# Kernel tuning notes

Hardware: AMD Instinct MI355X
Metric: run time of the kernel (lower is better)

Reference implementation:

```python
import jax, jax.numpy as jnp
import numpy as np

NUM_AGENTS = 50
NUM_SLOTS = 7
SLOT_DIM = 64
HIDDEN = 128
TOPK = 3
ITERS = 3


def _ln(x, eps=1e-5):
    m = x.mean(axis=-1, keepdims=True)
    v = ((x - m) ** 2).mean(axis=-1, keepdims=True)
    return (x - m) / jnp.sqrt(v + eps)


def setup_inputs() -> dict:
    key = jax.random.key(0)
    ks = jax.random.split(key, 20)
    r = lambda i, shape, s=0.05: jax.random.normal(ks[i], shape, dtype=jnp.float32) * s
    B = 32
    return {
        'images': jax.random.normal(ks[0], (B, 3, 32, 32), dtype=jnp.float32),
        'slot_noise': jax.random.normal(ks[1], (B, NUM_SLOTS, SLOT_DIM), dtype=jnp.float32),
        'enc_w0': r(2, (64, 3, 3, 3)), 'enc_b0': jnp.zeros((64,), jnp.float32),
        'enc_w': r(3, (3, 64, 64, 3, 3)), 'enc_b': jnp.zeros((3, 64), jnp.float32),
        'enc_wo': r(4, (256, 64, 3, 3)), 'enc_bo': jnp.zeros((256,), jnp.float32),
        'wk': r(5, (256, SLOT_DIM)), 'wv': r(6, (256, SLOT_DIM)), 'wq': r(7, (SLOT_DIM, SLOT_DIM)),
        'gru_wi': r(8, (SLOT_DIM, 3 * SLOT_DIM)), 'gru_wh': r(9, (SLOT_DIM, 3 * SLOT_DIM)),
        'gru_b': jnp.zeros((3 * SLOT_DIM,), jnp.float32),
        'mlp_w1': r(10, (SLOT_DIM, 128)), 'mlp_b1': jnp.zeros((128,), jnp.float32),
        'mlp_w2': r(11, (128, SLOT_DIM)), 'mlp_b2': jnp.zeros((SLOT_DIM,), jnp.float32),
        'slots_mu': r(12, (1, NUM_SLOTS, SLOT_DIM), 1.0),
        'slots_logsigma': jnp.zeros((1, NUM_SLOTS, SLOT_DIM), jnp.float32),
        'est_we': r(13, (NUM_AGENTS, SLOT_DIM, 32)), 'est_wd': r(14, (NUM_AGENTS, 32, SLOT_DIM)),
        'ag_win': r(15, (NUM_AGENTS, SLOT_DIM, 256)), 'ag_bin': jnp.zeros((NUM_AGENTS, 256), jnp.float32),
        'ag_wblk': r(16, (NUM_AGENTS, 3, 256, 256)), 'ag_bblk': jnp.zeros((NUM_AGENTS, 3, 256), jnp.float32),
        'ag_wout': r(17, (NUM_AGENTS, 256, HIDDEN)), 'ag_bout': jnp.zeros((NUM_AGENTS, HIDDEN), jnp.float32),
    }


def reference(images, slot_noise, enc_w0, enc_b0, enc_w, enc_b, enc_wo, enc_bo,
              wk, wv, wq, gru_wi, gru_wh, gru_b, mlp_w1, mlp_b1, mlp_w2, mlp_b2,
              slots_mu, slots_logsigma, est_we, est_wd,
              ag_win, ag_bin, ag_wblk, ag_bblk, ag_wout, ag_bout):
    conv = lambda x, w, b: jax.lax.conv_general_dilated(
        x, w, (1, 1), 'SAME', dimension_numbers=('NCHW', 'OIHW', 'NCHW')) + b[None, :, None, None]
    # ---- CNN encoder: 4 hidden conv layers + projection to 256 channels ----
    x = jax.nn.relu(conv(images, enc_w0, enc_b0))
    for i in range(enc_w.shape[0]):
        x = jax.nn.relu(conv(x, enc_w[i], enc_b[i]))
    feats = conv(x, enc_wo, enc_bo)                         # (B, 256, H, W)
    B, Df, H, W = feats.shape
    inputs = feats.transpose(0, 2, 3, 1).reshape(B, H * W, Df)  # (B, N, 256)
    inputs_n = _ln(inputs)
    k = inputs_n @ wk                                       # (B, N, Ds)
    v = inputs_n @ wv
    # ---- stochastic slot init ----
    slots = slots_mu + slot_noise * jnp.exp(slots_logsigma)  # (B, S, Ds)
    scale = SLOT_DIM ** -0.5
    # ---- slot attention, 3 iterations ----
    for _ in range(ITERS):
        prev = slots
        q = _ln(slots) @ wq * scale                         # (B, S, Ds)
        attn = jax.nn.softmax(jnp.einsum('bnd,bsd->bns', k, q), axis=-1) + 1e-8
        attn_w = attn / attn.sum(axis=1, keepdims=True)     # weighted mean over N
        updates = jnp.einsum('bns,bnd->bsd', attn_w, v)
        gi = updates @ gru_wi + gru_b
        gh = prev @ gru_wh
        zi, ri, ni = jnp.split(gi, 3, axis=-1)
        zh, rh, nh = jnp.split(gh, 3, axis=-1)
        z = jax.nn.sigmoid(zi + zh)
        rr = jax.nn.sigmoid(ri + rh)
        n = jnp.tanh(ni + rr * nh)
        slots = (1.0 - z) * n + z * prev
        slots = slots + (jax.nn.relu(_ln(slots) @ mlp_w1 + mlp_b1) @ mlp_w2 + mlp_b2)
    # ---- per-slot VAE-estimator scores (neg reconstruction error) ----
    lat = jnp.einsum('bsd,adz->bsaz', slots, est_we)        # (B, S, A, Z)
    recon = jnp.einsum('bsaz,azd->bsad', lat, est_wd)       # (B, S, A, Ds)
    scores = -((recon - slots[:, :, None, :]) ** 2).sum(axis=-1)  # (B, S, A)
    # ---- top-k agent selection per slot ----
    _, idx = jax.lax.top_k(scores, TOPK)                    # (B, S, K) int32
    ids = idx.reshape(-1)                                   # (T,) T = B*S*K
    tok = jnp.broadcast_to(slots[:, :, None, :], (B, NUM_SLOTS, TOPK, SLOT_DIM)).reshape(-1, SLOT_DIM)
    # ---- batched expert (residual MLP) dispatch via gathered params ----
    h = jax.nn.relu(jnp.einsum('td,tdh->th', tok, ag_win[ids]) + ag_bin[ids])  # (T, 256)
    for i in range(ag_wblk.shape[1]):
        h = jax.nn.relu(h + jnp.einsum('th,thg->tg', h, ag_wblk[ids, i]) + ag_bblk[ids, i])
    out = jnp.einsum('th,tho->to', h, ag_wout[ids]) + ag_bout[ids]             # (T, 128)
    hidden_labels = out.reshape(B, NUM_SLOTS * TOPK * HIDDEN)                  # concat mode: (B, 2688)
    return hidden_labels
```

## Files before the change

### kernel.cpp

```cpp
#include <hip/hip_runtime.h>
#include <hip/hip_bf16.h>
#include <math.h>

#define DEV __device__ __forceinline__

DEV double wred_sumd(double v) {
#pragma unroll
  for (int m = 1; m < 64; m <<= 1) v += __shfl_xor(v, m, 64);
  return v;
}

template <int CIN, bool RELU>
__global__ __launch_bounds__(256) void conv3x3_kernel(
    const float* __restrict__ in, const float* __restrict__ wgt,
    const float* __restrict__ bias, float* __restrict__ out,
    int cout_total, int cb_count) {
  constexpr int CHUNK = (CIN < 16) ? CIN : 16;
  __shared__ float s_in[6 * CHUNK * 35];
  __shared__ float s_w[CHUNK * 9 * 64];
  int bx = blockIdx.x;
  int cb = bx % cb_count;
  bx /= cb_count;
  int hb = bx & 7;
  int b = bx >> 3;
  int co_base = cb * 64;
  int t = threadIdx.x;
  int w_g = t & 7, co_g = (t >> 3) & 7, h_l = t >> 6;
  int h0 = hb * 4;
  int w0 = w_g * 4;
  float acc[8][4];
#pragma unroll
  for (int j = 0; j < 8; ++j)
#pragma unroll
    for (int ww = 0; ww < 4; ++ww) acc[j][ww] = 0.f;

  for (int cc = 0; cc < CIN; cc += CHUNK) {
    __syncthreads();
    for (int i = t; i < 6 * CHUNK * 32; i += 256) {
      int r = i / (CHUNK * 32);
      int c = (i >> 5) % CHUNK;
      int w = i & 31;
      int gh = h0 - 1 + r;
      float v = 0.f;
      if (gh >= 0 && gh < 32) v = in[((b * CIN + cc + c) * 32 + gh) * 32 + w];
      s_in[(r * CHUNK + c) * 35 + w + 1] = v;
    }
    for (int i = t; i < 6 * CHUNK; i += 256) {
      s_in[i * 35] = 0.f;
      s_in[i * 35 + 33] = 0.f;
    }
    for (int i = t; i < CHUNK * 9 * 64; i += 256) {
      int co = i / (CHUNK * 9);
      int rem = i % (CHUNK * 9);
      s_w[rem * 64 + co] = wgt[((co_base + co) * CIN + cc) * 9 + rem];
    }
    __syncthreads();
    for (int c = 0; c < CHUNK; ++c) {
#pragma unroll
      for (int kh = 0; kh < 3; ++kh) {
        const float* ip = &s_in[((h_l + kh) * CHUNK + c) * 35 + w0];
        float ivs[6];
#pragma unroll
        for (int j = 0; j < 6; ++j) ivs[j] = ip[j];
        const float* wp = &s_w[(c * 9 + kh * 3) * 64 + co_g * 8];
#pragma unroll
        for (int kw = 0; kw < 3; ++kw) {
          float4 wa = *(const float4*)(wp + kw * 64);
          float4 wb = *(const float4*)(wp + kw * 64 + 4);
          float wr[8] = {wa.x, wa.y, wa.z, wa.w, wb.x, wb.y, wb.z, wb.w};
#pragma unroll
          for (int j = 0; j < 8; ++j)
#pragma unroll
            for (int ww = 0; ww < 4; ++ww)
              acc[j][ww] = fmaf(ivs[kw + ww], wr[j], acc[j][ww]);
        }
      }
    }
  }
  int h = h0 + h_l;
#pragma unroll
  for (int j = 0; j < 8; ++j) {
    int co = co_base + co_g * 8 + j;
    float bv = bias[co];
    float4 o;
    o.x = acc[j][0] + bv;
    o.y = acc[j][1] + bv;
    o.z = acc[j][2] + bv;
    o.w = acc[j][3] + bv;
    if (RELU) {
      o.x = fmaxf(o.x, 0.f);
      o.y = fmaxf(o.y, 0.f);
      o.z = fmaxf(o.z, 0.f);
      o.w = fmaxf(o.w, 0.f);
    }
    *(float4*)(&out[((b * cout_total + co) * 32 + h) * 32 + w0]) = o;
  }
}

__global__ __launch_bounds__(256) void conv5_ln_kv_fused(
    const float* __restrict__ in,
    const float* __restrict__ wgt,
    const float* __restrict__ bias,
    const float* __restrict__ wk, const float* __restrict__ wv,
    float* __restrict__ kout, float* __restrict__ vout) {
  int bp = blockIdx.x;
  int b = bp >> 6, pt = bp & 63;
  int h = pt >> 1, w0 = (pt & 1) * 16;
  int t = threadIdx.x;
  int px = t & 15, cg = t >> 4;

  __shared__ float s_w[2 * 9 * 256];
  __shared__ float s_in[2][3][20];
  __shared__ float s_red[16][17];
  __shared__ float s_m[16], s_isd[16];
  __shared__ float s_xn[16][257];

  float acc[16];
#pragma unroll
  for (int j = 0; j < 16; ++j) acc[j] = 0.f;

  for (int cc = 0; cc < 64; cc += 2) {
    __syncthreads();
    for (int i = t; i < 2 * 9 * 256; i += 256) {
      int co = i & 255;
      int rem = i >> 8;
      int c = rem / 9, k = rem % 9;
      s_w[(c * 9 + k) * 256 + co] = wgt[(co * 64 + cc + c) * 9 + k];
    }
    for (int i = t; i < 2 * 3 * 18; i += 256) {
      int c = i / 54;
      int r = (i / 18) % 3;
      int cw = i % 18;
      int gh = h + r - 1;
      int gw = w0 + cw - 1;
      float v = 0.f;
      if (gh >= 0 && gh < 32 && gw >= 0 && gw < 32)
        v = in[((b * 64 + c + cc) * 32 + gh) * 32 + gw];
      s_in[c][r][cw] = v;
    }
    __syncthreads();
#pragma unroll
    for (int c = 0; c < 2; ++c) {
#pragma unroll
      for (int kh = 0; kh < 3; ++kh) {
        float iv[3];
#pragma unroll
        for (int kw = 0; kw < 3; ++kw) iv[kw] = s_in[c][kh][px + kw];
        const float* wp = &s_w[(c * 9 + kh * 3) * 256 + cg * 16];
#pragma unroll
        for (int kw = 0; kw < 3; ++kw) {
#pragma unroll
          for (int j = 0; j < 16; ++j)
            acc[j] = fmaf(iv[kw], wp[kw * 256 + j], acc[j]);
        }
      }
    }
  }
#pragma unroll
  for (int j = 0; j < 16; ++j) acc[j] += bias[cg * 16 + j];
  float psum = 0.f;
#pragma unroll
  for (int j = 0; j < 16; ++j) psum += acc[j];
  s_red[px][cg] = psum;
  __syncthreads();
  if (t < 16) {
    float m = 0.f;
    for (int g = 0; g < 16; ++g) m += s_red[t][g];
    s_m[t] = m * (1.f / 256.f);
  }
  __syncthreads();
  float m = s_m[px];
  float vp = 0.f;
#pragma unroll
  for (int j = 0; j < 16; ++j) {
    float dv = acc[j] - m;
    vp += dv * dv;
  }
  s_red[px][cg] = vp;
  __syncthreads();
  if (t < 16) {
    float v = 0.f;
    for (int g = 0; g < 16; ++g) v += s_red[t][g];
    s_isd[t] = 1.f / sqrtf(v * (1.f / 256.f) + 1e-5f);
  }
  __syncthreads();
  float isd = s_isd[px];
#pragma unroll
  for (int j = 0; j < 16; ++j) s_xn[px][cg * 16 + j] = (acc[j] - m) * isd;
  __syncthreads();
  const float* wb = (cg < 8) ? wk : wv;
  int d0 = (cg & 7) * 8;
  float a2[8];
#pragma unroll
  for (int j = 0; j < 8; ++j) a2[j] = 0.f;
  for (int c = 0; c < 256; ++c) {
    float xv = s_xn[px][c];
    const float* wr = &wb[c * 64 + d0];
#pragma unroll
    for (int j = 0; j < 8; ++j) a2[j] = fmaf(xv, wr[j], a2[j]);
  }
  int p = h * 32 + w0 + px;
  float* ob = (cg < 8) ? kout : vout;
#pragma unroll
  for (int j = 0; j < 8; ++j) ob[(b * 1024 + p) * 64 + d0 + j] = a2[j];
}

__global__ __launch_bounds__(64) void slot_init(
    const float* __restrict__ mu, const float* __restrict__ logsig,
    const float* __restrict__ noise, const float* __restrict__ wq,
    double* __restrict__ slots, double* __restrict__ qbuf) {
  int bs = blockIdx.x;
  int d = threadIdx.x;
  int sr = bs % 7;
  __shared__ double ln[64], red[64];
  double s = (double)mu[sr * 64 + d] +
             (double)noise[bs * 64 + d] * exp((double)logsig[sr * 64 + d]);
  slots[bs * 64 + d] = s;
  red[d] = s;
  __syncthreads();
  for (int st = 32; st > 0; st >>= 1) {
    if (d < st) red[d] += red[d + st];
    __syncthreads();
  }
  double m = red[0] * (1.0 / 64.0);
  __syncthreads();
  double dv = s - m;
  red[d] = dv * dv;
  __syncthreads();
  for (int st = 32; st > 0; st >>= 1) {
    if (d < st) red[d] += red[d + st];
    __syncthreads();
  }
  double isd = 1.0 / sqrt(red[0] * (1.0 / 64.0) + 1e-5);
  __syncthreads();
  ln[d] = dv * isd;
  __syncthreads();
  double q = 0.0;
  for (int dd = 0; dd < 64; ++dd) q += ln[dd] * (double)wq[dd * 64 + d];
  qbuf[bs * 64 + d] = q * 0.125;
}

__global__ __launch_bounds__(256) void attn_softmax(
    const float* __restrict__ kbuf, const double* __restrict__ qbuf,
    double* __restrict__ attw) {
  int idx = blockIdx.x * 256 + threadIdx.x;
  if (idx >= 32 * 1024) return;
  int b = idx >> 10;
  int n = idx & 1023;
  double l[7];
  for (int s = 0; s < 7; ++s) {
    double acc = 0.0;
    for (int d = 0; d < 64; ++d)
      acc += (double)kbuf[idx * 64 + d] * qbuf[(b * 7 + s) * 64 + d];
    l[s] = acc;
  }
  double mx = l[0];
  for (int s = 1; s < 7; ++s) mx = fmax(mx, l[s]);
  double sum = 0.0;
  for (int s = 0; s < 7; ++s) {
    l[s] = exp(l[s] - mx);
    sum += l[s];
  }
  double inv = 1.0 / sum;
  for (int s = 0; s < 7; ++s)
    attw[(size_t)(b * 7 + s) * 1024 + n] = l[s] * inv + 1e-8;
}

__global__ __launch_bounds__(256) void attn_update_slot(
    const double* __restrict__ attw, const float* __restrict__ vbuf,
    const float* __restrict__ gwi, const float* __restrict__ gwh,
    const float* __restrict__ gb, const float* __restrict__ w1,
    const float* __restrict__ b1, const float* __restrict__ w2,
    const float* __restrict__ b2, const float* __restrict__ wq,
    double* __restrict__ slots, double* __restrict__ qbuf) {
  int bs = blockIdx.x;
  int b = bs / 7;
  int t = threadIdx.x;
  int d = t & 63, q = t >> 6;
  __shared__ double s_aw[1024];
  __shared__ double part[4][64];
  __shared__ double red256[256];
  __shared__ double s_u[64], s_p[64], s_ln[64], s_h[128];
  for (int i = t; i < 1024; i += 256) s_aw[i] = attw[(size_t)bs * 1024 + i];
  __syncthreads();
  double ps = 0.0;
#pragma unroll
  for (int k = 0; k < 4; ++k) ps += s_aw[q * 256 + k * 64 + d];
  red256[t] = ps;
  double acc = 0.0;
  const float* vb = vbuf + ((size_t)(b * 1024 + q * 256)) * 64 + d;
  for (int n = 0; n < 256; ++n)
    acc += s_aw[q * 256 + n] * (double)vb[(size_t)n * 64];
  part[q][d] = acc;
  __syncthreads();
  for (int st = 128; st > 0; st >>= 1) {
    if (t < st) red256[t] += red256[t + st];
    __syncthreads();
  }
  double asum = red256[0];
  if (t < 64) {
    double u = ((part[0][d] + part[1][d]) + part[2][d]) + part[3][d];
    s_u[d] = u / asum;
    s_p[d] = slots[bs * 64 + d];
  }
  __syncthreads();
  if (t >= 64) return;
  double giz = (double)gb[d], gir = (double)gb[64 + d], gin = (double)gb[128 + d];
  double ghz = 0.0, ghr = 0.0, ghn = 0.0;
  for (int dd = 0; dd < 64; ++dd) {
    double uu = s_u[dd], pp = s_p[dd];
    giz += uu * (double)gwi[dd * 192 + d];
    gir += uu * (double)gwi[dd * 192 + 64 + d];
    gin += uu * (double)gwi[dd * 192 + 128 + d];
    ghz += pp * (double)gwh[dd * 192 + d];
    ghr += pp * (double)gwh[dd * 192 + 64 + d];
    ghn += pp * (double)gwh[dd * 192 + 128 + d];
  }
  double z = 1.0 / (1.0 + exp(-(giz + ghz)));
  double r = 1.0 / (1.0 + exp(-(gir + ghr)));
  double nn = tanh(gin + r * ghn);
  double sv = (1.0 - z) * nn + z * s_p[d];
  double m = wred_sumd(sv) * (1.0 / 64.0);
  double dv = sv - m;
  double var = wred_sumd(dv * dv) * (1.0 / 64.0);
  s_ln[d] = dv / sqrt(var + 1e-5);
  double h0 = (double)b1[d], h1 = (double)b1[64 + d];
  for (int dd = 0; dd < 64; ++dd) {
    double lv = s_ln[dd];
    h0 += lv * (double)w1[dd * 128 + d];
    h1 += lv * (double)w1[dd * 128 + 64 + d];
  }
  s_h[d] = fmax(h0, 0.0);
  s_h[64 + d] = fmax(h1, 0.0);
  double o = (double)b2[d];
  for (int e = 0; e < 128; ++e) o += s_h[e] * (double)w2[e * 64 + d];
  double s2 = sv + o;
  slots[bs * 64 + d] = s2;
  double m2 = wred_sumd(s2) * (1.0 / 64.0);
  double dv2 = s2 - m2;
  double var2 = wred_sumd(dv2 * dv2) * (1.0 / 64.0);
  s_ln[d] = dv2 / sqrt(var2 + 1e-5);
  double qv = 0.0;
  for (int dd = 0; dd < 64; ++dd) qv += s_ln[dd] * (double)wq[dd * 64 + d];
  qbuf[bs * 64 + d] = qv * 0.125;
}

__global__ __launch_bounds__(256) void scores_naive(
    const double* __restrict__ slots, const float* __restrict__ we,
    const float* __restrict__ wd, double* __restrict__ sc) {
  int idx = blockIdx.x * 256 + threadIdx.x;
  if (idx >= 224 * 50) return;
  int a = idx % 50, bs = idx / 50;
  double lat[32];
  for (int z = 0; z < 32; ++z) {
    double acc = 0.0;
    for (int dd = 0; dd < 64; ++dd)
      acc += slots[bs * 64 + dd] * (double)we[(a * 64 + dd) * 32 + z];
    lat[z] = acc;
  }
  double sum = 0.0;
  for (int dd = 0; dd < 64; ++dd) {
    double rec = 0.0;
    for (int z = 0; z < 32; ++z) rec += lat[z] * (double)wd[(a * 32 + z) * 64 + dd];
    double df = rec - slots[bs * 64 + dd];
    sum += df * df;
  }
  sc[idx] = -sum;
}

__global__ __launch_bounds__(256) void topk_naive(const double* __restrict__ sc,
                                                  int* __restrict__ topk) {
  int bs = blockIdx.x * 256 + threadIdx.x;
  if (bs >= 224) return;
  int chosen[3];
  for (int r = 0; r < 3; ++r) {
    double best = -1e300;
    int bi = -1;
    for (int a = 0; a < 50; ++a) {
      bool skip = false;
      for (int rr = 0; rr < r; ++rr)
        if (chosen[rr] == a) skip = true;
      if (skip) continue;
      double v = sc[bs * 50 + a];
      if (v > best) {
        best = v;
        bi = a;
      }
    }
    chosen[r] = bi;
    topk[bs * 3 + r] = bi;
  }
}

__global__ __launch_bounds__(256) void expert_naive(
    const int* __restrict__ topk, const double* __restrict__ slots,
    const float* __restrict__ win, const float* __restrict__ bin,
    const float* __restrict__ wblk, const float* __restrict__ bblk,
    const float* __restrict__ wout, const float* __restrict__ bout,
    float* __restrict__ outp) {
  int ti = blockIdx.x;
  int a = topk[ti];
  int bs = ti / 3;
  int t = threadIdx.x;
  __shared__ double tok[64], ha[256], hb[256];
  if (t < 64) tok[t] = slots[bs * 64 + t];
  __syncthreads();
  double acc = (double)bin[a * 256 + t];
  for (int dd = 0; dd < 64; ++dd)
    acc += tok[dd] * (double)win[(a * 64 + dd) * 256 + t];
  ha[t] = fmax(acc, 0.0);
  __syncthreads();
  double* cur = ha;
  double* nxt = hb;
  for (int i = 0; i < 3; ++i) {
    double a2 = cur[t] + (double)bblk[(a * 3 + i) * 256 + t];
    for (int hh = 0; hh < 256; ++hh)
      a2 += cur[hh] * (double)wblk[((a * 3 + i) * 256 + hh) * 256 + t];
    nxt[t] = fmax(a2, 0.0);
    __syncthreads();
    double* tmp = cur;
    cur = nxt;
    nxt = tmp;
  }
  if (t < 128) {
    double a3 = (double)bout[a * 128 + t];
    for (int hh = 0; hh < 256; ++hh)
      a3 += cur[hh] * (double)wout[(a * 256 + hh) * 128 + t];
    outp[ti * 128 + t] = (float)a3;
  }
}

extern "C" void kernel_launch(void* const* d_in, const int* in_sizes, int n_in,
                              void* d_out, int out_size, void* d_ws,
                              size_t ws_size, hipStream_t stream) {
  (void)in_sizes; (void)n_in; (void)out_size; (void)ws_size;
  const float* images = (const float*)d_in[0];
  const float* noise = (const float*)d_in[1];
  const float* enc_w0 = (const float*)d_in[2];
  const float* enc_b0 = (const float*)d_in[3];
  const float* enc_w = (const float*)d_in[4];
  const float* enc_b = (const float*)d_in[5];
  const float* enc_wo = (const float*)d_in[6];
  const float* enc_bo = (const float*)d_in[7];
  const float* wk = (const float*)d_in[8];
  const float* wv = (const float*)d_in[9];
  const float* wq = (const float*)d_in[10];
  const float* gru_wi = (const float*)d_in[11];
  const float* gru_wh = (const float*)d_in[12];
  const float* gru_b = (const float*)d_in[13];
  const float* mlp_w1 = (const float*)d_in[14];
  const float* mlp_b1 = (const float*)d_in[15];
  const float* mlp_w2 = (const float*)d_in[16];
  const float* mlp_b2 = (const float*)d_in[17];
  const float* mu = (const float*)d_in[18];
  const float* logsig = (const float*)d_in[19];
  const float* est_we = (const float*)d_in[20];
  const float* est_wd = (const float*)d_in[21];
  const float* ag_win = (const float*)d_in[22];
  const float* ag_bin = (const float*)d_in[23];
  const float* ag_wblk = (const float*)d_in[24];
  const float* ag_bblk = (const float*)d_in[25];
  const float* ag_wout = (const float*)d_in[26];
  const float* ag_bout = (const float*)d_in[27];

  double* dws = (double*)d_ws;
  double* slots = dws;
  double* qbuf = slots + 14336;
  double* upd = qbuf + 14336;
  double* attw = upd + 14336;
  double* sc = attw + 229376;
  int* topk = (int*)(sc + 11200);
  float* xA = (float*)(topk + 1024);
  float* xB = xA + 2097152;
  float* vbuf = xB + 2097152;

  conv3x3_kernel<3, true><<<256, 256, 0, stream>>>(images, enc_w0, enc_b0, xA, 64, 1);
  conv3x3_kernel<64, true><<<256, 256, 0, stream>>>(xA, enc_w, enc_b, xB, 64, 1);
  conv3x3_kernel<64, true><<<256, 256, 0, stream>>>(xB, enc_w + 36864, enc_b + 64, xA, 64, 1);
  conv3x3_kernel<64, true><<<256, 256, 0, stream>>>(xA, enc_w + 73728, enc_b + 128, xB, 64, 1);
  conv5_ln_kv_fused<<<2048, 256, 0, stream>>>(xB, enc_wo, enc_bo, wk, wv, xA, vbuf);
  slot_init<<<224, 64, 0, stream>>>(mu, logsig, noise, wq, slots, qbuf);
  for (int it = 0; it < 3; ++it) {
    attn_softmax<<<128, 256, 0, stream>>>(xA, qbuf, attw);
    attn_update_slot<<<224, 256, 0, stream>>>(attw, vbuf, gru_wi, gru_wh,
                                              gru_b, mlp_w1, mlp_b1, mlp_w2,
                                              mlp_b2, wq, slots, qbuf);
  }
  scores_naive<<<44, 256, 0, stream>>>(slots, est_we, est_wd, sc);
  topk_naive<<<1, 256, 0, stream>>>(sc, topk);
  expert_naive<<<672, 256, 0, stream>>>(topk, slots, ag_win, ag_bin, ag_wblk,
                                        ag_bblk, ag_wout, ag_bout,
                                        (float*)d_out);
}
```

Before: 1.755 ms.

## Coalesce conv5 weight loads, stage q in LDS, widen slot-update blocks

The conv5 weight staging now reads global weights contiguously per output channel and stores them into a padded LDS layout (stride 257). This trades bank conflicts on the store for coalesced global reads. attn_softmax caches the per-batch queries in shared memory and loads each key row as float4 vectors, avoiding repeated strided global reads. attn_update_slot uses 512 threads so the attention-weighted value sum is split eight ways, which shortens each thread's serial loop but adds reduction and sync cost.

```diff
diff --git a/kernel.cpp b/kernel.cpp
--- a/kernel.cpp
+++ b/kernel.cpp
@@ -109,7 +109,7 @@
   int t = threadIdx.x;
   int px = t & 15, cg = t >> 4;
 
-  __shared__ float s_w[2 * 9 * 256];
+  __shared__ float s_w[18 * 257];
   __shared__ float s_in[2][3][20];
   __shared__ float s_red[16][17];
   __shared__ float s_m[16], s_isd[16];
@@ -121,11 +121,9 @@
 
   for (int cc = 0; cc < 64; cc += 2) {
     __syncthreads();
-    for (int i = t; i < 2 * 9 * 256; i += 256) {
-      int co = i & 255;
-      int rem = i >> 8;
-      int c = rem / 9, k = rem % 9;
-      s_w[(c * 9 + k) * 256 + co] = wgt[(co * 64 + cc + c) * 9 + k];
+    for (int i = t; i < 256 * 18; i += 256) {
+      int co = i / 18, rem = i % 18;
+      s_w[rem * 257 + co] = wgt[co * 576 + cc * 9 + rem];
     }
     for (int i = t; i < 2 * 3 * 18; i += 256) {
       int c = i / 54;
@@ -146,12 +144,12 @@
         float iv[3];
 #pragma unroll
         for (int kw = 0; kw < 3; ++kw) iv[kw] = s_in[c][kh][px + kw];
-        const float* wp = &s_w[(c * 9 + kh * 3) * 256 + cg * 16];
+        const float* wp = &s_w[(c * 9 + kh * 3) * 257 + cg * 16];
 #pragma unroll
         for (int kw = 0; kw < 3; ++kw) {
 #pragma unroll
           for (int j = 0; j < 16; ++j)
-            acc[j] = fmaf(iv[kw], wp[kw * 256 + j], acc[j]);
+            acc[j] = fmaf(iv[kw], wp[kw * 257 + j], acc[j]);
         }
       }
     }
@@ -243,30 +241,48 @@
 __global__ __launch_bounds__(256) void attn_softmax(
     const float* __restrict__ kbuf, const double* __restrict__ qbuf,
     double* __restrict__ attw) {
-  int idx = blockIdx.x * 256 + threadIdx.x;
-  if (idx >= 32 * 1024) return;
-  int b = idx >> 10;
-  int n = idx & 1023;
+  int bx = blockIdx.x;
+  int b = bx >> 2;
+  int n0 = (bx & 3) * 256;
+  int t = threadIdx.x;
+  int n = n0 + t;
+  __shared__ double s_q[448];
+  for (int i = t; i < 448; i += 256) s_q[i] = qbuf[b * 448 + i];
+  __syncthreads();
+  float4 kr[16];
+  const float4* kp = (const float4*)(kbuf + ((size_t)(b * 1024 + n)) * 64);
+#pragma unroll
+  for (int i = 0; i < 16; ++i) kr[i] = kp[i];
   double l[7];
+#pragma unroll
   for (int s = 0; s < 7; ++s) {
     double acc = 0.0;
-    for (int d = 0; d < 64; ++d)
-      acc += (double)kbuf[idx * 64 + d] * qbuf[(b * 7 + s) * 64 + d];
+    const double* qs = &s_q[s * 64];
+#pragma unroll
+    for (int i = 0; i < 16; ++i) {
+      acc += (double)kr[i].x * qs[i * 4 + 0];
+      acc += (double)kr[i].y * qs[i * 4 + 1];
+      acc += (double)kr[i].z * qs[i * 4 + 2];
+      acc += (double)kr[i].w * qs[i * 4 + 3];
+    }
     l[s] = acc;
   }
   double mx = l[0];
+#pragma unroll
   for (int s = 1; s < 7; ++s) mx = fmax(mx, l[s]);
   double sum = 0.0;
+#pragma unroll
   for (int s = 0; s < 7; ++s) {
     l[s] = exp(l[s] - mx);
     sum += l[s];
   }
   double inv = 1.0 / sum;
+#pragma unroll
   for (int s = 0; s < 7; ++s)
     attw[(size_t)(b * 7 + s) * 1024 + n] = l[s] * inv + 1e-8;
 }
 
-__global__ __launch_bounds__(256) void attn_update_slot(
+__global__ __launch_bounds__(512) void attn_update_slot(
     const double* __restrict__ attw, const float* __restrict__ vbuf,
     const float* __restrict__ gwi, const float* __restrict__ gwh,
     const float* __restrict__ gb, const float* __restrict__ w1,
@@ -278,28 +294,26 @@
   int t = threadIdx.x;
   int d = t & 63, q = t >> 6;
   __shared__ double s_aw[1024];
-  __shared__ double part[4][64];
-  __shared__ double red256[256];
+  __shared__ double part[8][64];
+  __shared__ double red[512];
   __shared__ double s_u[64], s_p[64], s_ln[64], s_h[128];
-  for (int i = t; i < 1024; i += 256) s_aw[i] = attw[(size_t)bs * 1024 + i];
-  __syncthreads();
-  double ps = 0.0;
-#pragma unroll
-  for (int k = 0; k < 4; ++k) ps += s_aw[q * 256 + k * 64 + d];
-  red256[t] = ps;
+  for (int i = t; i < 1024; i += 512) s_aw[i] = attw[(size_t)bs * 1024 + i];
+  __syncthreads();
+  red[t] = s_aw[t] + s_aw[t + 512];
   double acc = 0.0;
-  const float* vb = vbuf + ((size_t)(b * 1024 + q * 256)) * 64 + d;
-  for (int n = 0; n < 256; ++n)
-    acc += s_aw[q * 256 + n] * (double)vb[(size_t)n * 64];
+  const float* vb = vbuf + ((size_t)(b * 1024 + q * 128)) * 64 + d;
+  for (int nn = 0; nn < 128; ++nn)
+    acc += s_aw[q * 128 + nn] * (double)vb[(size_t)nn * 64];
   part[q][d] = acc;
   __syncthreads();
-  for (int st = 128; st > 0; st >>= 1) {
-    if (t < st) red256[t] += red256[t + st];
-    __syncthreads();
-  }
-  double asum = red256[0];
+  for (int st = 256; st > 0; st >>= 1) {
+    if (t < st) red[t] += red[t + st];
+    __syncthreads();
+  }
+  double asum = red[0];
   if (t < 64) {
-    double u = ((part[0][d] + part[1][d]) + part[2][d]) + part[3][d];
+    double u = ((part[0][d] + part[1][d]) + (part[2][d] + part[3][d])) +
+               ((part[4][d] + part[5][d]) + (part[6][d] + part[7][d]));
     s_u[d] = u / asum;
     s_p[d] = slots[bs * 64 + d];
   }
@@ -318,8 +332,8 @@
   }
   double z = 1.0 / (1.0 + exp(-(giz + ghz)));
   double r = 1.0 / (1.0 + exp(-(gir + ghr)));
-  double nn = tanh(gin + r * ghn);
-  double sv = (1.0 - z) * nn + z * s_p[d];
+  double nn2 = tanh(gin + r * ghn);
+  double sv = (1.0 - z) * nn2 + z * s_p[d];
   double m = wred_sumd(sv) * (1.0 / 64.0);
   double dv = sv - m;
   double var = wred_sumd(dv * dv) * (1.0 / 64.0);
@@ -482,7 +496,7 @@
   slot_init<<<224, 64, 0, stream>>>(mu, logsig, noise, wq, slots, qbuf);
   for (int it = 0; it < 3; ++it) {
     attn_softmax<<<128, 256, 0, stream>>>(xA, qbuf, attw);
-    attn_update_slot<<<224, 256, 0, stream>>>(attw, vbuf, gru_wi, gru_wh,
+    attn_update_slot<<<224, 512, 0, stream>>>(attw, vbuf, gru_wi, gru_wh,
                                               gru_b, mlp_w1, mlp_b1, mlp_w2,
                                               mlp_b2, wq, slots, qbuf);
   }
```

New measurement: 1.478 ms. 15.8% less time.
